# Kernel optimization log

Measured on AMD Instinct MI355X. Metric: run time of the kernel, lower is better.

The kernel has to match this reference:

```python
import jax, jax.numpy as jnp
import numpy as np

B, C_IN, C_OUT, T, R, CO = 8, 64, 64, 32, 32, 32


def setup_inputs() -> dict:
    key = jax.random.key(0)
    ks = jax.random.split(key, 8)
    scale = 1.0 / np.sqrt(C_IN)  # nn.Linear default uniform(-1/sqrt(in), 1/sqrt(in))
    w = lambda k: jax.random.uniform(k, (C_OUT, C_IN), jnp.float32, -scale, scale)
    return {
        "x": jax.random.normal(ks[0], (B, C_IN, T, R, CO), jnp.float32),
        "w_self": w(ks[1]),
        "w_tp": w(ks[2]),
        "w_tm": w(ks[3]),
        "w_rp": w(ks[4]),
        "w_rm": w(ks[5]),
        "w_cp": w(ks[6]),
        "w_cm": w(ks[7]),
    }


def _proj(v, w):
    # v: [B, t, r, c, C_in], w: [C_out, C_in] (nn.Linear layout)
    return jnp.einsum('btrci,oi->btrco', v, w)


def _shift_pad(a, axis, front):
    # pad 1 slice at front (True) or back (False) along `axis` of a 5-D tensor
    pads = [(0, 0)] * 5
    pads[axis] = (1, 0) if front else (0, 1)
    return jnp.pad(a, pads)


def reference(x, w_self, w_tp, w_tm, w_rp, w_rm, w_cp, w_cm):
    xp = jnp.transpose(x, (0, 2, 3, 4, 1))  # [B, T, R, Co, C_in]
    out = _proj(xp, w_self)
    if xp.shape[1] > 1:
        out = out + _shift_pad(_proj(xp[:, :-1], w_tp), 1, True)
        out = out + _shift_pad(_proj(xp[:, 1:], w_tm), 1, False)
    if xp.shape[2] > 1:
        out = out + _shift_pad(_proj(xp[:, :, :-1], w_rp), 2, True)
        out = out + _shift_pad(_proj(xp[:, :, 1:], w_rm), 2, False)
    if xp.shape[3] > 1:
        out = out + _shift_pad(_proj(xp[:, :, :, :-1], w_cp), 3, True)
        out = out + _shift_pad(_proj(xp[:, :, :, 1:], w_cm), 3, False)
    return jnp.transpose(out, (0, 4, 1, 2, 3))  # [B, C_out, T, R, Co]
```

## Files before the change

kernel.cpp:

```cpp
#include <hip/hip_runtime.h>


#define SB 32768
#define CIN 64
#define COUT 64
#define NB 8

typedef short s16x8 __attribute__((ext_vector_type(8)));
typedef __bf16 bf16x8 __attribute__((ext_vector_type(8)));
typedef float f32x4 __attribute__((ext_vector_type(4)));

__device__ __forceinline__ unsigned f2bf(float f) {
    unsigned u = __float_as_uint(f);
    u += 0x7FFFu + ((u >> 16) & 1u);
    return u >> 16;
}
__device__ __forceinline__ unsigned pk2(float lo, float hi) {
    return f2bf(lo) | (f2bf(hi) << 16);
}

__global__ __launch_bounds__(256) void wprep_kernel(const float* __restrict__ w0,
                            const float* __restrict__ w1, const float* __restrict__ w2,
                            const float* __restrict__ w3, const float* __restrict__ w4,
                            const float* __restrict__ w5, const float* __restrict__ w6,
                            unsigned short* __restrict__ ws) {
    int tap = blockIdx.x;
    int tid = threadIdx.x;
    const float* w = (tap == 0) ? w0 : (tap == 1) ? w1 : (tap == 2) ? w2
                   : (tap == 3) ? w3 : (tap == 4) ? w4 : (tap == 5) ? w5 : w6;
    unsigned p[8];
#pragma unroll
    for (int j = 0; j < 8; ++j)
        p[j] = pk2(w[tid * 16 + 2 * j], w[tid * 16 + 2 * j + 1]);
    uint4* dp = (uint4*)(ws + tap * 4096 + tid * 16);
    dp[0] = make_uint4(p[0], p[1], p[2], p[3]);
    dp[1] = make_uint4(p[4], p[5], p[6], p[7]);
}

__global__ __launch_bounds__(256) void conv_kernel(const float* __restrict__ x,
                                                   const unsigned short* __restrict__ wq,
                                                   float* __restrict__ out) {
    __shared__ uint4 alds[2560];
    int bid = blockIdx.x;
    int b = bid >> 7;
    int sblk = (bid & 127) << 8;
    int tid = threadIdx.x;
    const float* xb = x + (size_t)b * CIN * SB;

    {
        int rl = 32 + tid;
        const float* xp = xb + sblk + tid;
#pragma unroll
        for (int c = 0; c < 4; ++c) {
            unsigned pk[8];
#pragma unroll
            for (int u = 0; u < 8; ++u)
                pk[u] = pk2(xp[(size_t)(c * 16 + 2 * u) * SB],
                            xp[(size_t)(c * 16 + 2 * u + 1) * SB]);
            alds[rl * 8 + ((2 * c) ^ (rl & 7))] = make_uint4(pk[0], pk[1], pk[2], pk[3]);
            alds[rl * 8 + ((2 * c + 1) ^ (rl & 7))] = make_uint4(pk[4], pk[5], pk[6], pk[7]);
        }
    }
    {
        int hrow = tid & 63;
        int rl = (hrow < 32) ? hrow : hrow + 256;
        int s = sblk - 32 + rl;
        s = max(0, min(SB - 1, s));
        int ic = tid >> 6;
        const float* xp = xb + s + (size_t)(ic * 16) * SB;
        unsigned pk[8];
#pragma unroll
        for (int u = 0; u < 8; ++u)
            pk[u] = pk2(xp[(size_t)(2 * u) * SB], xp[(size_t)(2 * u + 1) * SB]);
        alds[rl * 8 + ((2 * ic) ^ (rl & 7))] = make_uint4(pk[0], pk[1], pk[2], pk[3]);
        alds[rl * 8 + ((2 * ic + 1) ^ (rl & 7))] = make_uint4(pk[4], pk[5], pk[6], pk[7]);
    }
    __syncthreads();

    int lane = tid & 63;
    int wv = tid >> 6;
    int lo = lane & 15;
    int quad = lane >> 4;
    int sbase = sblk + wv * 64;
    int t = sblk >> 10;

    f32x4 acc[4][4];
#pragma unroll
    for (int mt = 0; mt < 4; ++mt)
#pragma unroll
        for (int nt = 0; nt < 4; ++nt)
            acc[mt][nt] = (f32x4){0.f, 0.f, 0.f, 0.f};

    int r_m[4], c_m[4], rl[4];
#pragma unroll
    for (int mt = 0; mt < 4; ++mt) {
        int s = sbase + mt * 16 + lo;
        r_m[mt] = (s >> 5) & 31;
        c_m[mt] = s & 31;
        rl[mt] = s - sblk + 32;
    }

    auto load_b = [&](const unsigned short* wt, int ks, int nt) -> bf16x8 {
        const unsigned short* bp = wt + (nt * 16 + lo) * 64 + ks * 32 + quad * 8;
        return __builtin_bit_cast(bf16x8, *(const s16x8*)bp);
    };

    auto run_tap_lds = [&](int tap, int d, const bool ok[4]) {
        const unsigned short* wt = wq + tap * 4096;
#pragma unroll
        for (int ks = 0; ks < 2; ++ks) {
            bf16x8 bf[4];
#pragma unroll
            for (int nt = 0; nt < 4; ++nt) bf[nt] = load_b(wt, ks, nt);
            int j = ks * 4 + quad;
#pragma unroll
            for (int mt = 0; mt < 4; ++mt) {
                int row = rl[mt] + d;
                s16x8 raw = *((const s16x8*)alds + row * 8 + (j ^ (row & 7)));
                s16x8 zz = {0, 0, 0, 0, 0, 0, 0, 0};
                raw = ok[mt] ? raw : zz;
                bf16x8 af = __builtin_bit_cast(bf16x8, raw);
#pragma unroll
                for (int nt = 0; nt < 4; ++nt)
                    acc[mt][nt] = __builtin_amdgcn_mfma_f32_16x16x32_bf16(af, bf[nt], acc[mt][nt], 0, 0, 0);
            }
        }
    };

    auto run_tap_gather = [&](int tap, int d) {
        const unsigned short* wt = wq + tap * 4096;
#pragma unroll
        for (int ks = 0; ks < 2; ++ks) {
            bf16x8 bf[4];
#pragma unroll
            for (int nt = 0; nt < 4; ++nt) bf[nt] = load_b(wt, ks, nt);
            const float* gp = xb + (size_t)(ks * 32 + quad * 8) * SB + d;
#pragma unroll
            for (int mt = 0; mt < 4; ++mt) {
                const float* ap = gp + sbase + mt * 16 + lo;
                unsigned pk[4];
#pragma unroll
                for (int u = 0; u < 4; ++u)
                    pk[u] = pk2(ap[(size_t)(2 * u) * SB], ap[(size_t)(2 * u + 1) * SB]);
                uint4 v = make_uint4(pk[0], pk[1], pk[2], pk[3]);
                bf16x8 af = __builtin_bit_cast(bf16x8, v);
#pragma unroll
                for (int nt = 0; nt < 4; ++nt)
                    acc[mt][nt] = __builtin_amdgcn_mfma_f32_16x16x32_bf16(af, bf[nt], acc[mt][nt], 0, 0, 0);
            }
        }
    };

    {
        bool ok_all[4] = {true, true, true, true};
        run_tap_lds(0, 0, ok_all);
    }
    if (t > 0)  run_tap_gather(1, -1024);
    if (t < 31) run_tap_gather(2, 1024);
    {
        bool ok[4];
#pragma unroll
        for (int mt = 0; mt < 4; ++mt) ok[mt] = (r_m[mt] > 0);
        run_tap_lds(3, -32, ok);
#pragma unroll
        for (int mt = 0; mt < 4; ++mt) ok[mt] = (r_m[mt] < 31);
        run_tap_lds(4, 32, ok);
#pragma unroll
        for (int mt = 0; mt < 4; ++mt) ok[mt] = (c_m[mt] > 0);
        run_tap_lds(5, -1, ok);
#pragma unroll
        for (int mt = 0; mt < 4; ++mt) ok[mt] = (c_m[mt] < 31);
        run_tap_lds(6, 1, ok);
    }

#pragma unroll
    for (int mt = 0; mt < 4; ++mt) {
#pragma unroll
        for (int nt = 0; nt < 4; ++nt) {
            int o = nt * 16 + lo;
            size_t off = ((size_t)(b * COUT + o)) * SB + sbase + mt * 16 + quad * 4;
            *(f32x4*)(out + off) = acc[mt][nt];
        }
    }
}

__global__ void fallback_kernel(const float* __restrict__ x,
                                const float* __restrict__ w0, const float* __restrict__ w1,
                                const float* __restrict__ w2, const float* __restrict__ w3,
                                const float* __restrict__ w4, const float* __restrict__ w5,
                                const float* __restrict__ w6,
                                float* __restrict__ out) {
    int bid = blockIdx.x;
    int b = bid >> 11;
    int og = (bid >> 7) & 15;
    int sblk = (bid & 127) << 8;
    int tid = threadIdx.x;
    __shared__ float wl[7][4][64];
    const float* wp[7] = {w0, w1, w2, w3, w4, w5, w6};
    for (int k = tid; k < 7 * 4 * 64; k += 256) {
        int tap = k >> 8, oo = (k >> 6) & 3, i = k & 63;
        wl[tap][oo][i] = wp[tap][(og * 4 + oo) * 64 + i];
    }
    __syncthreads();
    int s = sblk + tid;
    int t = s >> 10, r = (s >> 5) & 31, c = s & 31;
    const float* xb = x + (size_t)b * CIN * SB + s;
    float a0 = 0, a1 = 0, a2 = 0, a3 = 0;
    for (int i = 0; i < 64; ++i) {
        const float* xi = xb + (size_t)i * SB;
        float vs = xi[0];
        float vtp = (t > 0) ? xi[-1024] : 0.f;
        float vtm = (t < 31) ? xi[1024] : 0.f;
        float vrp = (r > 0) ? xi[-32] : 0.f;
        float vrm = (r < 31) ? xi[32] : 0.f;
        float vcp = (c > 0) ? xi[-1] : 0.f;
        float vcm = (c < 31) ? xi[1] : 0.f;
        a0 += wl[0][0][i] * vs + wl[1][0][i] * vtp + wl[2][0][i] * vtm + wl[3][0][i] * vrp + wl[4][0][i] * vrm + wl[5][0][i] * vcp + wl[6][0][i] * vcm;
        a1 += wl[0][1][i] * vs + wl[1][1][i] * vtp + wl[2][1][i] * vtm + wl[3][1][i] * vrp + wl[4][1][i] * vrm + wl[5][1][i] * vcp + wl[6][1][i] * vcm;
        a2 += wl[0][2][i] * vs + wl[1][2][i] * vtp + wl[2][2][i] * vtm + wl[3][2][i] * vrp + wl[4][2][i] * vrm + wl[5][2][i] * vcp + wl[6][2][i] * vcm;
        a3 += wl[0][3][i] * vs + wl[1][3][i] * vtp + wl[2][3][i] * vtm + wl[3][3][i] * vrp + wl[4][3][i] * vrm + wl[5][3][i] * vcp + wl[6][3][i] * vcm;
    }
    size_t obase = ((size_t)b * COUT + og * 4) * SB + s;
    out[obase] = a0;
    out[obase + SB] = a1;
    out[obase + 2 * (size_t)SB] = a2;
    out[obase + 3 * (size_t)SB] = a3;
}

extern "C" void kernel_launch(void* const* d_in, const int* in_sizes, int n_in,
                              void* d_out, int out_size, void* d_ws, size_t ws_size,
                              hipStream_t stream) {
    const float* x = (const float*)d_in[0];
    const float* w0 = (const float*)d_in[1];
    const float* w1 = (const float*)d_in[2];
    const float* w2 = (const float*)d_in[3];
    const float* w3 = (const float*)d_in[4];
    const float* w4 = (const float*)d_in[5];
    const float* w5 = (const float*)d_in[6];
    const float* w6 = (const float*)d_in[7];
    float* out = (float*)d_out;

    size_t need = (size_t)7 * 4096 * 2;
    if (d_ws != nullptr && ws_size >= need) {
        unsigned short* wsp = (unsigned short*)d_ws;
        wprep_kernel<<<7, 256, 0, stream>>>(w0, w1, w2, w3, w4, w5, w6, wsp);
        conv_kernel<<<1024, 256, 0, stream>>>(x, wsp, out);
    } else {
        fallback_kernel<<<8 * 16 * 128, 256, 0, stream>>>(x, w0, w1, w2, w3, w4, w5, w6, out);
    }
}
```

Measured before the change: 158.5 us.

## Pre-transpose input to channel-last bf16 workspace and convolve from global memory

Adds a prep kernel that converts x to bf16 in a position-major, channel-contiguous layout in the workspace, folded together with the weight conversion. A new conv kernel then reads neighbour rows for all seven taps straight from global memory (L2/cache) with MFMA, without staging halos in LDS. The aim is to drop the LDS halo staging and repeated fp32 conversion from the main kernel. The cost is an extra full write and read of a bf16 copy of x (about 32 MB), and the path needs a much larger workspace.

```diff
diff --git a/kernel.cpp b/kernel.cpp
--- a/kernel.cpp
+++ b/kernel.cpp
@@ -35,6 +35,147 @@
     uint4* dp = (uint4*)(ws + tap * 4096 + tid * 16);
     dp[0] = make_uint4(p[0], p[1], p[2], p[3]);
     dp[1] = make_uint4(p[4], p[5], p[6], p[7]);
+}
+
+__global__ __launch_bounds__(256) void prep_kernel(const float* __restrict__ x,
+                            const float* __restrict__ w0, const float* __restrict__ w1,
+                            const float* __restrict__ w2, const float* __restrict__ w3,
+                            const float* __restrict__ w4, const float* __restrict__ w5,
+                            const float* __restrict__ w6,
+                            unsigned short* __restrict__ ws) {
+    int bid = blockIdx.x;
+    int tid = threadIdx.x;
+    if (bid >= 1024) {
+        int tap = bid - 1024;
+        const float* w = (tap == 0) ? w0 : (tap == 1) ? w1 : (tap == 2) ? w2
+                       : (tap == 3) ? w3 : (tap == 4) ? w4 : (tap == 5) ? w5 : w6;
+        unsigned p[8];
+#pragma unroll
+        for (int j = 0; j < 8; ++j)
+            p[j] = pk2(w[tid * 16 + 2 * j], w[tid * 16 + 2 * j + 1]);
+        uint4* dp = (uint4*)(ws + tap * 4096 + tid * 16);
+        dp[0] = make_uint4(p[0], p[1], p[2], p[3]);
+        dp[1] = make_uint4(p[4], p[5], p[6], p[7]);
+        return;
+    }
+    __shared__ uint4 l[2048];
+    int lbid = ((bid & 7) << 7) | (bid >> 3);
+    int b = lbid >> 7;
+    int sblk = (lbid & 127) << 8;
+    unsigned short* xq = ws + 7 * 4096;
+    const float* xp = x + (size_t)b * CIN * SB + sblk + tid;
+#pragma unroll
+    for (int c = 0; c < 4; ++c) {
+        unsigned pk[8];
+#pragma unroll
+        for (int u = 0; u < 8; ++u)
+            pk[u] = pk2(xp[(size_t)(c * 16 + 2 * u) * SB],
+                        xp[(size_t)(c * 16 + 2 * u + 1) * SB]);
+        l[tid * 8 + ((2 * c) ^ (tid & 7))] = make_uint4(pk[0], pk[1], pk[2], pk[3]);
+        l[tid * 8 + ((2 * c + 1) ^ (tid & 7))] = make_uint4(pk[4], pk[5], pk[6], pk[7]);
+    }
+    __syncthreads();
+    uint4* dst = (uint4*)(xq + ((size_t)b * SB + sblk) * 64);
+#pragma unroll
+    for (int k = 0; k < 8; ++k) {
+        int idx = k * 256 + tid;
+        int row = idx >> 3;
+        int col = idx & 7;
+        dst[idx] = l[row * 8 + (col ^ (row & 7))];
+    }
+}
+
+__global__ __launch_bounds__(256) void conv2_kernel(const unsigned short* __restrict__ xq,
+                                                    const unsigned short* __restrict__ wq,
+                                                    float* __restrict__ out) {
+    int bid = blockIdx.x;
+    int lbid = ((bid & 7) << 7) | (bid >> 3);
+    int b = lbid >> 7;
+    int sblk = (lbid & 127) << 8;
+    int tid = threadIdx.x;
+    int lane = tid & 63;
+    int wv = tid >> 6;
+    int lo = lane & 15;
+    int quad = lane >> 4;
+    int sbase = sblk + wv * 64;
+    int t = sblk >> 10;
+    const unsigned short* xb = xq + (size_t)b * (CIN * SB);
+
+    f32x4 acc[4][4];
+#pragma unroll
+    for (int mt = 0; mt < 4; ++mt)
+#pragma unroll
+        for (int nt = 0; nt < 4; ++nt)
+            acc[mt][nt] = (f32x4){0.f, 0.f, 0.f, 0.f};
+
+    int s_m[4], r_m[4], c_m[4];
+#pragma unroll
+    for (int mt = 0; mt < 4; ++mt) {
+        int s = sbase + mt * 16 + lo;
+        s_m[mt] = s;
+        r_m[mt] = (s >> 5) & 31;
+        c_m[mt] = s & 31;
+    }
+
+    auto load_b = [&](const unsigned short* wt, int ks, int nt) -> bf16x8 {
+        const unsigned short* bp = wt + (nt * 16 + lo) * 64 + ks * 32 + quad * 8;
+        return __builtin_bit_cast(bf16x8, *(const s16x8*)bp);
+    };
+
+    auto run_tap = [&](int tap, int d, const bool ok[4]) {
+        const unsigned short* wt = wq + tap * 4096;
+#pragma unroll
+        for (int ks = 0; ks < 2; ++ks) {
+            bf16x8 bf[4];
+#pragma unroll
+            for (int nt = 0; nt < 4; ++nt) bf[nt] = load_b(wt, ks, nt);
+#pragma unroll
+            for (int mt = 0; mt < 4; ++mt) {
+                int s = s_m[mt] + d;
+                s = s < 0 ? 0 : s;
+                s = s > SB - 1 ? SB - 1 : s;
+                s16x8 raw = *(const s16x8*)(xb + (size_t)s * 64 + ks * 32 + quad * 8);
+                s16x8 zz = {0, 0, 0, 0, 0, 0, 0, 0};
+                raw = ok[mt] ? raw : zz;
+                bf16x8 af = __builtin_bit_cast(bf16x8, raw);
+#pragma unroll
+                for (int nt = 0; nt < 4; ++nt)
+                    acc[mt][nt] = __builtin_amdgcn_mfma_f32_16x16x32_bf16(af, bf[nt], acc[mt][nt], 0, 0, 0);
+            }
+        }
+    };
+
+    {
+        bool ok_all[4] = {true, true, true, true};
+        run_tap(0, 0, ok_all);
+        if (t > 0)  run_tap(1, -1024, ok_all);
+        if (t < 31) run_tap(2, 1024, ok_all);
+    }
+    {
+        bool ok[4];
+#pragma unroll
+        for (int mt = 0; mt < 4; ++mt) ok[mt] = (r_m[mt] > 0);
+        run_tap(3, -32, ok);
+#pragma unroll
+        for (int mt = 0; mt < 4; ++mt) ok[mt] = (r_m[mt] < 31);
+        run_tap(4, 32, ok);
+#pragma unroll
+        for (int mt = 0; mt < 4; ++mt) ok[mt] = (c_m[mt] > 0);
+        run_tap(5, -1, ok);
+#pragma unroll
+        for (int mt = 0; mt < 4; ++mt) ok[mt] = (c_m[mt] < 31);
+        run_tap(6, 1, ok);
+    }
+
+#pragma unroll
+    for (int mt = 0; mt < 4; ++mt) {
+#pragma unroll
+        for (int nt = 0; nt < 4; ++nt) {
+            int o = nt * 16 + lo;
+            size_t off = ((size_t)(b * COUT + o)) * SB + sbase + mt * 16 + quad * 4;
+            *(f32x4*)(out + off) = acc[mt][nt];
+        }
+    }
 }
 
 __global__ __launch_bounds__(256) void conv_kernel(const float* __restrict__ x,
@@ -240,8 +381,13 @@
     const float* w6 = (const float*)d_in[7];
     float* out = (float*)d_out;
 
-    size_t need = (size_t)7 * 4096 * 2;
-    if (d_ws != nullptr && ws_size >= need) {
+    size_t need_w = (size_t)7 * 4096 * 2;
+    size_t need_full = need_w + (size_t)NB * CIN * SB * 2;
+    if (d_ws != nullptr && ws_size >= need_full) {
+        unsigned short* wsp = (unsigned short*)d_ws;
+        prep_kernel<<<1031, 256, 0, stream>>>(x, w0, w1, w2, w3, w4, w5, w6, wsp);
+        conv2_kernel<<<1024, 256, 0, stream>>>(wsp + 7 * 4096, wsp, out);
+    } else if (d_ws != nullptr && ws_size >= need_w) {
         unsigned short* wsp = (unsigned short*)d_ws;
         wprep_kernel<<<7, 256, 0, stream>>>(w0, w1, w2, w3, w4, w5, w6, wsp);
         conv_kernel<<<1024, 256, 0, stream>>>(x, wsp, out);
```

After: 178.9 us. +12.9%, slower.
